# Kernel optimization log

Hardware: AMD Instinct MI355X
Metric: run time of the kernel (lower is better)

Reference implementation:

```python
import jax, jax.numpy as jnp
import numpy as np

IN_CH = 128
INTER = max(IN_CH // 8, 1)  # 16

def setup_inputs() -> dict:
    key = jax.random.key(0)
    ks = jax.random.split(key, 10)
    B, C, D, H, W = 2, IN_CH, 16, 24, 24
    s = 1.0 / np.sqrt(C)
    so = 1.0 / np.sqrt(INTER)
    return {
        "x":  jax.random.normal(ks[0], (B, C, D, H, W), dtype=jnp.float32),
        "Wq": jax.random.normal(ks[1], (INTER, C), dtype=jnp.float32) * s,
        "bq": jax.random.normal(ks[2], (INTER,), dtype=jnp.float32) * 0.01,
        "Wk": jax.random.normal(ks[3], (INTER, C), dtype=jnp.float32) * s,
        "bk": jax.random.normal(ks[4], (INTER,), dtype=jnp.float32) * 0.01,
        "Wv": jax.random.normal(ks[5], (INTER, C), dtype=jnp.float32) * s,
        "bv": jax.random.normal(ks[6], (INTER,), dtype=jnp.float32) * 0.01,
        "Wo": jax.random.normal(ks[7], (C, INTER), dtype=jnp.float32) * so,
        "bo": jax.random.normal(ks[8], (C,), dtype=jnp.float32) * 0.01,
        "gamma": jnp.zeros((1,), dtype=jnp.float32) + 0.5,  # nonzero so attn path is exercised
    }

def reference(x, Wq, bq, Wk, bk, Wv, bv, Wo, bo, gamma):
    B, C, D, H, W = x.shape
    N = D * H * W
    xf = x.reshape(B, C, N)  # flatten spatial
    # 1x1x1 conv == per-voxel channel matmul
    q = jnp.einsum('ic,bcn->bin', Wq, xf) + bq[None, :, None]  # [B,I,N]
    k = jnp.einsum('ic,bcn->bin', Wk, xf) + bk[None, :, None]
    v = jnp.einsum('ic,bcn->bin', Wv, xf) + bv[None, :, None]
    # attention[b,n,m] = sum_i q[b,i,n] k[b,i,m]; softmax over keys m
    attn = jax.nn.softmax(jnp.einsum('bin,bim->bnm', q, k), axis=-1)
    # out[b,c,n] = sum_m v[b,c,m] attn[b,n,m]
    out = jnp.einsum('bim,bnm->bin', v, attn)  # [B,I,N]
    out = jnp.einsum('ci,bin->bcn', Wo, out) + bo[None, :, None]
    out = out.reshape(B, C, D, H, W)
    return gamma[0] * out + x
```

## Files before the change

kernel.cpp:

```cpp
#include <hip/hip_runtime.h>

#define C_CH 128
#define I_CH 16
#define NVOX 9216
#define BATCH 2
#define LOG2E 1.44269504088896340736f

typedef unsigned short ushort_t;
typedef unsigned int uint_t;
typedef short bf16x8 __attribute__((ext_vector_type(8)));
typedef float f32x4 __attribute__((ext_vector_type(4)));

static __device__ inline ushort_t f2bf_rne(float x) {
    uint_t u = __builtin_bit_cast(uint_t, x);
    u = (u + 0x7FFFu + ((u >> 16) & 1u)) >> 16;
    return (ushort_t)u;
}

static __device__ inline float fast_exp2(float x) {
#if __has_builtin(__builtin_amdgcn_exp2f)
    return __builtin_amdgcn_exp2f(x);
#else
    return exp2f(x);
#endif
}

__global__ __launch_bounds__(256) void qkv_kernel(
    const float* __restrict__ x,
    const float* __restrict__ Wq, const float* __restrict__ bq,
    const float* __restrict__ Wk, const float* __restrict__ bk,
    const float* __restrict__ Wv, const float* __restrict__ bv,
    ushort_t* __restrict__ qb, ushort_t* __restrict__ kb,
    ushort_t* __restrict__ vT)
{
    __shared__ float xs[C_CH][64];
    __shared__ float ws[3][I_CH][C_CH];

    const int blk = blockIdx.x;
    const int b   = blk / (NVOX / 64);
    const int n0  = (blk % (NVOX / 64)) * 64;
    const int t   = threadIdx.x;

    {
        float4* wsq = (float4*)&ws[0][0][0];
        float4* wsk = (float4*)&ws[1][0][0];
        float4* wsv = (float4*)&ws[2][0][0];
        wsq[t]       = ((const float4*)Wq)[t];
        wsq[t + 256] = ((const float4*)Wq)[t + 256];
        wsk[t]       = ((const float4*)Wk)[t];
        wsk[t + 256] = ((const float4*)Wk)[t + 256];
        wsv[t]       = ((const float4*)Wv)[t];
        wsv[t + 256] = ((const float4*)Wv)[t + 256];
    }

    const float* xb = x + (size_t)b * C_CH * NVOX;
    #pragma unroll
    for (int rep = 0; rep < 8; ++rep) {
        int idx4 = rep * 256 + t;
        int c    = idx4 >> 4;
        int n4   = (idx4 & 15) << 2;
        *(float4*)&xs[c][n4] = *(const float4*)(xb + (size_t)c * NVOX + n0 + n4);
    }
    __syncthreads();

    const int n  = t & 63;
    const int iw = t >> 6;
    const int i0 = iw * 4;

    float aq[4] = {0.f,0.f,0.f,0.f};
    float ak[4] = {0.f,0.f,0.f,0.f};
    float av[4] = {0.f,0.f,0.f,0.f};

    #pragma unroll 2
    for (int c = 0; c < C_CH; c += 4) {
        float xv0 = xs[c + 0][n];
        float xv1 = xs[c + 1][n];
        float xv2 = xs[c + 2][n];
        float xv3 = xs[c + 3][n];
        #pragma unroll
        for (int j = 0; j < 4; ++j) {
            float4 w4;
            w4 = *(const float4*)&ws[0][i0 + j][c];
            aq[j] = fmaf(w4.x, xv0, fmaf(w4.y, xv1, fmaf(w4.z, xv2, fmaf(w4.w, xv3, aq[j]))));
            w4 = *(const float4*)&ws[1][i0 + j][c];
            ak[j] = fmaf(w4.x, xv0, fmaf(w4.y, xv1, fmaf(w4.z, xv2, fmaf(w4.w, xv3, ak[j]))));
            w4 = *(const float4*)&ws[2][i0 + j][c];
            av[j] = fmaf(w4.x, xv0, fmaf(w4.y, xv1, fmaf(w4.z, xv2, fmaf(w4.w, xv3, av[j]))));
        }
    }

    const size_t vox = (size_t)b * NVOX + n0 + n;
    ushort4 qv, kv;
    qv.x = f2bf_rne((aq[0] + bq[i0+0]) * LOG2E);
    qv.y = f2bf_rne((aq[1] + bq[i0+1]) * LOG2E);
    qv.z = f2bf_rne((aq[2] + bq[i0+2]) * LOG2E);
    qv.w = f2bf_rne((aq[3] + bq[i0+3]) * LOG2E);
    kv.x = f2bf_rne(ak[0] + bk[i0+0]); kv.y = f2bf_rne(ak[1] + bk[i0+1]);
    kv.z = f2bf_rne(ak[2] + bk[i0+2]); kv.w = f2bf_rne(ak[3] + bk[i0+3]);
    *(ushort4*)(qb + vox * I_CH + i0) = qv;
    *(ushort4*)(kb + vox * I_CH + i0) = kv;

    const int nl = n0 + n;
    #pragma unroll
    for (int j = 0; j < 4; ++j)
        vT[((size_t)b * I_CH + i0 + j) * NVOX + nl] = f2bf_rne(av[j] + bv[i0+j]);
}

__global__ __launch_bounds__(512) void attn_kernel(
    const ushort_t* __restrict__ qb, const ushort_t* __restrict__ kb,
    const ushort_t* __restrict__ vT,
    const float* __restrict__ Wo, const float* __restrict__ bo,
    const float* __restrict__ gamma, const float* __restrict__ x,
    float* __restrict__ out)
{
    __shared__ float po[4][32][18];
    __shared__ float lsh[8][33];
    __shared__ float aot[16][40];
    __shared__ float wo_s[C_CH][17];

    const int tid  = threadIdx.x;
    const int w    = tid >> 6;
    const int lane = tid & 63;
    const int l16  = lane & 15;
    const int quad = lane >> 4;

    {
        const int c  = tid >> 2;
        const int i4 = (tid & 3) * 4;
        float4 wv = *(const float4*)(Wo + c * I_CH + i4);
        wo_s[c][i4 + 0] = wv.x; wo_s[c][i4 + 1] = wv.y;
        wo_s[c][i4 + 2] = wv.z; wo_s[c][i4 + 3] = wv.w;
    }

    const int qvox0 = blockIdx.x * 32;
    const int b     = qvox0 / NVOX;
    const int nloc0 = qvox0 - b * NVOX;

    bf16x8 qf0 = (bf16x8)0, qf1 = (bf16x8)0;
    if (quad < 2) {
        qf0 = __builtin_bit_cast(bf16x8,
              *(const int4*)(qb + (size_t)(qvox0 + l16) * I_CH + quad * 8));
        qf1 = __builtin_bit_cast(bf16x8,
              *(const int4*)(qb + (size_t)(qvox0 + 16 + l16) * I_CH + quad * 8));
    }

    const int p0     = ((l16 >> 2) << 3) + (l16 & 3);
    const int mchunk = w * (NVOX / 8);
    const ushort_t* kp = kb + ((size_t)b * NVOX + mchunk + p0) * I_CH + (quad & 1) * 8;
    const ushort_t* vp = vT + ((size_t)b * I_CH + l16) * NVOX + mchunk + quad * 8;

    f32x4 O0 = {0.f,0.f,0.f,0.f}, O1 = {0.f,0.f,0.f,0.f};
    f32x4 L0 = {0.f,0.f,0.f,0.f}, L1 = {0.f,0.f,0.f,0.f};
    const f32x4 Z = {0.f,0.f,0.f,0.f};
    int4 onesi; onesi.x = onesi.y = onesi.z = onesi.w = 0x3F803F80;
    const bf16x8 ones = __builtin_bit_cast(bf16x8, onesi);

    for (int it = 0; it < NVOX / 8 / 64; ++it) {
        int4 ka0a = *(const int4*)(kp);
        int4 ka1a = *(const int4*)(kp + 4 * I_CH);
        int4 vaa  = *(const int4*)(vp);
        int4 ka0b = *(const int4*)(kp + 32 * I_CH);
        int4 ka1b = *(const int4*)(kp + 36 * I_CH);
        int4 vab  = *(const int4*)(vp + 32);
        kp += 64 * I_CH;
        vp += 64;

        f32x4 s00 = __builtin_amdgcn_mfma_f32_16x16x32_bf16(
            __builtin_bit_cast(bf16x8, ka0a), qf0, Z, 0, 0, 0);
        f32x4 s01 = __builtin_amdgcn_mfma_f32_16x16x32_bf16(
            __builtin_bit_cast(bf16x8, ka1a), qf0, Z, 0, 0, 0);
        f32x4 s10 = __builtin_amdgcn_mfma_f32_16x16x32_bf16(
            __builtin_bit_cast(bf16x8, ka0a), qf1, Z, 0, 0, 0);
        f32x4 s11 = __builtin_amdgcn_mfma_f32_16x16x32_bf16(
            __builtin_bit_cast(bf16x8, ka1a), qf1, Z, 0, 0, 0);

        f32x4 t00 = __builtin_amdgcn_mfma_f32_16x16x32_bf16(
            __builtin_bit_cast(bf16x8, ka0b), qf0, Z, 0, 0, 0);
        f32x4 t01 = __builtin_amdgcn_mfma_f32_16x16x32_bf16(
            __builtin_bit_cast(bf16x8, ka1b), qf0, Z, 0, 0, 0);
        f32x4 t10 = __builtin_amdgcn_mfma_f32_16x16x32_bf16(
            __builtin_bit_cast(bf16x8, ka0b), qf1, Z, 0, 0, 0);
        f32x4 t11 = __builtin_amdgcn_mfma_f32_16x16x32_bf16(
            __builtin_bit_cast(bf16x8, ka1b), qf1, Z, 0, 0, 0);

        {
            float p00 = fast_exp2(s00.x), p01 = fast_exp2(s00.y);
            float p02 = fast_exp2(s00.z), p03 = fast_exp2(s00.w);
            float p10 = fast_exp2(s01.x), p11 = fast_exp2(s01.y);
            float p12 = fast_exp2(s01.z), p13 = fast_exp2(s01.w);
            uint_t d0 = __builtin_amdgcn_perm(__builtin_bit_cast(uint_t, p01),
                                              __builtin_bit_cast(uint_t, p00), 0x07060302u);
            uint_t d1 = __builtin_amdgcn_perm(__builtin_bit_cast(uint_t, p03),
                                              __builtin_bit_cast(uint_t, p02), 0x07060302u);
            uint_t d2 = __builtin_amdgcn_perm(__builtin_bit_cast(uint_t, p11),
                                              __builtin_bit_cast(uint_t, p10), 0x07060302u);
            uint_t d3 = __builtin_amdgcn_perm(__builtin_bit_cast(uint_t, p13),
                                              __builtin_bit_cast(uint_t, p12), 0x07060302u);
            int4 pbi = make_int4((int)d0, (int)d1, (int)d2, (int)d3);
            bf16x8 pb = __builtin_bit_cast(bf16x8, pbi);
            O0 = __builtin_amdgcn_mfma_f32_16x16x32_bf16(
                __builtin_bit_cast(bf16x8, vaa), pb, O0, 0, 0, 0);
            L0 = __builtin_amdgcn_mfma_f32_16x16x32_bf16(ones, pb, L0, 0, 0, 0);
        }
        {
            float p00 = fast_exp2(s10.x), p01 = fast_exp2(s10.y);
            float p02 = fast_exp2(s10.z), p03 = fast_exp2(s10.w);
            float p10 = fast_exp2(s11.x), p11 = fast_exp2(s11.y);
            float p12 = fast_exp2(s11.z), p13 = fast_exp2(s11.w);
            uint_t d0 = __builtin_amdgcn_perm(__builtin_bit_cast(uint_t, p01),
                                              __builtin_bit_cast(uint_t, p00), 0x07060302u);
            uint_t d1 = __builtin_amdgcn_perm(__builtin_bit_cast(uint_t, p03),
                                              __builtin_bit_cast(uint_t, p02), 0x07060302u);
            uint_t d2 = __builtin_amdgcn_perm(__builtin_bit_cast(uint_t, p11),
                                              __builtin_bit_cast(uint_t, p10), 0x07060302u);
            uint_t d3 = __builtin_amdgcn_perm(__builtin_bit_cast(uint_t, p13),
                                              __builtin_bit_cast(uint_t, p12), 0x07060302u);
            int4 pbi = make_int4((int)d0, (int)d1, (int)d2, (int)d3);
            bf16x8 pb = __builtin_bit_cast(bf16x8, pbi);
            O1 = __builtin_amdgcn_mfma_f32_16x16x32_bf16(
                __builtin_bit_cast(bf16x8, vaa), pb, O1, 0, 0, 0);
            L1 = __builtin_amdgcn_mfma_f32_16x16x32_bf16(ones, pb, L1, 0, 0, 0);
        }
        {
            float p00 = fast_exp2(t00.x), p01 = fast_exp2(t00.y);
            float p02 = fast_exp2(t00.z), p03 = fast_exp2(t00.w);
            float p10 = fast_exp2(t01.x), p11 = fast_exp2(t01.y);
            float p12 = fast_exp2(t01.z), p13 = fast_exp2(t01.w);
            uint_t d0 = __builtin_amdgcn_perm(__builtin_bit_cast(uint_t, p01),
                                              __builtin_bit_cast(uint_t, p00), 0x07060302u);
            uint_t d1 = __builtin_amdgcn_perm(__builtin_bit_cast(uint_t, p03),
                                              __builtin_bit_cast(uint_t, p02), 0x07060302u);
            uint_t d2 = __builtin_amdgcn_perm(__builtin_bit_cast(uint_t, p11),
                                              __builtin_bit_cast(uint_t, p10), 0x07060302u);
            uint_t d3 = __builtin_amdgcn_perm(__builtin_bit_cast(uint_t, p13),
                                              __builtin_bit_cast(uint_t, p12), 0x07060302u);
            int4 pbi = make_int4((int)d0, (int)d1, (int)d2, (int)d3);
            bf16x8 pb = __builtin_bit_cast(bf16x8, pbi);
            O0 = __builtin_amdgcn_mfma_f32_16x16x32_bf16(
                __builtin_bit_cast(bf16x8, vab), pb, O0, 0, 0, 0);
            L0 = __builtin_amdgcn_mfma_f32_16x16x32_bf16(ones, pb, L0, 0, 0, 0);
        }
        {
            float p00 = fast_exp2(t10.x), p01 = fast_exp2(t10.y);
            float p02 = fast_exp2(t10.z), p03 = fast_exp2(t10.w);
            float p10 = fast_exp2(t11.x), p11 = fast_exp2(t11.y);
            float p12 = fast_exp2(t11.z), p13 = fast_exp2(t11.w);
            uint_t d0 = __builtin_amdgcn_perm(__builtin_bit_cast(uint_t, p01),
                                              __builtin_bit_cast(uint_t, p00), 0x07060302u);
            uint_t d1 = __builtin_amdgcn_perm(__builtin_bit_cast(uint_t, p03),
                                              __builtin_bit_cast(uint_t, p02), 0x07060302u);
            uint_t d2 = __builtin_amdgcn_perm(__builtin_bit_cast(uint_t, p11),
                                              __builtin_bit_cast(uint_t, p10), 0x07060302u);
            uint_t d3 = __builtin_amdgcn_perm(__builtin_bit_cast(uint_t, p13),
                                              __builtin_bit_cast(uint_t, p12), 0x07060302u);
            int4 pbi = make_int4((int)d0, (int)d1, (int)d2, (int)d3);
            bf16x8 pb = __builtin_bit_cast(bf16x8, pbi);
            O1 = __builtin_amdgcn_mfma_f32_16x16x32_bf16(
                __builtin_bit_cast(bf16x8, vab), pb, O1, 0, 0, 0);
            L1 = __builtin_amdgcn_mfma_f32_16x16x32_bf16(ones, pb, L1, 0, 0, 0);
        }
    }

    if (w < 4) {
        #pragma unroll
        for (int r = 0; r < 4; ++r) {
            po[w][quad * 4 + r][l16]      = O0[r];
            po[w][16 + quad * 4 + r][l16] = O1[r];
        }
    }
    if (quad == 0) { lsh[w][l16] = L0.x; lsh[w][16 + l16] = L1.x; }
    __syncthreads();

    if (w >= 4) {
        #pragma unroll
        for (int r = 0; r < 4; ++r) {
            po[w - 4][quad * 4 + r][l16]      += O0[r];
            po[w - 4][16 + quad * 4 + r][l16] += O1[r];
        }
    }
    __syncthreads();

    {
        const int q32 = tid & 31;
        const int i   = tid >> 5;
        const int row = (q32 >> 4) * 16 + i;
        const int col = q32 & 15;
        float v = 0.f, l = 0.f;
        #pragma unroll
        for (int ww = 0; ww < 4; ++ww) v += po[ww][row][col];
        #pragma unroll
        for (int ww = 0; ww < 8; ++ww) l += lsh[ww][q32];
        aot[i][q32] = v / l;
    }
    __syncthreads();

    const float g  = gamma[0];
    const int   c  = tid >> 2;
    const int   qh = (tid & 3) * 8;

    float acc[8];
    {
        const float b0 = bo[c];
        #pragma unroll
        for (int q = 0; q < 8; ++q) acc[q] = b0;
    }
    #pragma unroll
    for (int i = 0; i < 16; ++i) {
        const float wv = wo_s[c][i];
        float4 a0 = *(const float4*)&aot[i][qh];
        float4 a1 = *(const float4*)&aot[i][qh + 4];
        acc[0] = fmaf(wv, a0.x, acc[0]); acc[1] = fmaf(wv, a0.y, acc[1]);
        acc[2] = fmaf(wv, a0.z, acc[2]); acc[3] = fmaf(wv, a0.w, acc[3]);
        acc[4] = fmaf(wv, a1.x, acc[4]); acc[5] = fmaf(wv, a1.y, acc[5]);
        acc[6] = fmaf(wv, a1.z, acc[6]); acc[7] = fmaf(wv, a1.w, acc[7]);
    }

    const size_t gi = ((size_t)b * C_CH + c) * NVOX + nloc0 + qh;
    float4 x0 = *(const float4*)(x + gi);
    float4 x1 = *(const float4*)(x + gi + 4);
    float4 o0, o1;
    o0.x = fmaf(g, acc[0], x0.x); o0.y = fmaf(g, acc[1], x0.y);
    o0.z = fmaf(g, acc[2], x0.z); o0.w = fmaf(g, acc[3], x0.w);
    o1.x = fmaf(g, acc[4], x1.x); o1.y = fmaf(g, acc[5], x1.y);
    o1.z = fmaf(g, acc[6], x1.z); o1.w = fmaf(g, acc[7], x1.w);
    *(float4*)(out + gi)     = o0;
    *(float4*)(out + gi + 4) = o1;
}

extern "C" void kernel_launch(void* const* d_in, const int* in_sizes, int n_in,
                              void* d_out, int out_size, void* d_ws, size_t ws_size,
                              hipStream_t stream) {
    const float* x     = (const float*)d_in[0];
    const float* Wq    = (const float*)d_in[1];
    const float* bq    = (const float*)d_in[2];
    const float* Wk    = (const float*)d_in[3];
    const float* bk    = (const float*)d_in[4];
    const float* Wv    = (const float*)d_in[5];
    const float* bv    = (const float*)d_in[6];
    const float* Wo    = (const float*)d_in[7];
    const float* bo    = (const float*)d_in[8];
    const float* gamma = (const float*)d_in[9];
    float* out = (float*)d_out;

    ushort_t* qb = (ushort_t*)d_ws;
    ushort_t* kb = qb + (size_t)BATCH * NVOX * I_CH;
    ushort_t* vT = kb + (size_t)BATCH * NVOX * I_CH;

    hipLaunchKernelGGL(qkv_kernel, dim3(BATCH * NVOX / 64), dim3(256), 0, stream,
                       x, Wq, bq, Wk, bk, Wv, bv, qb, kb, vT);
    hipLaunchKernelGGL(attn_kernel, dim3(BATCH * NVOX / 32), dim3(512), 0, stream,
                       qb, kb, vT, Wo, bo, gamma, x, out);
}
```

Before: 130.0 us.

## Split key range across 16 waves and shrink QKV projection tiles

```diff
diff --git a/kernel.cpp b/kernel.cpp
--- a/kernel.cpp
+++ b/kernel.cpp
@@ -33,88 +33,70 @@
     ushort_t* __restrict__ qb, ushort_t* __restrict__ kb,
     ushort_t* __restrict__ vT)
 {
-    __shared__ float xs[C_CH][64];
-    __shared__ float ws[3][I_CH][C_CH];
-
-    const int blk = blockIdx.x;
-    const int b   = blk / (NVOX / 64);
-    const int n0  = (blk % (NVOX / 64)) * 64;
-    const int t   = threadIdx.x;
+    __shared__ float ws[3][I_CH][132];
+    __shared__ float xs[C_CH][I_CH];
+
+    const int t    = threadIdx.x;
+    const int vox0 = blockIdx.x * 16;
+    const int b    = vox0 / NVOX;
+    const int n0   = vox0 - b * NVOX;
 
     {
-        float4* wsq = (float4*)&ws[0][0][0];
-        float4* wsk = (float4*)&ws[1][0][0];
-        float4* wsv = (float4*)&ws[2][0][0];
-        wsq[t]       = ((const float4*)Wq)[t];
-        wsq[t + 256] = ((const float4*)Wq)[t + 256];
-        wsk[t]       = ((const float4*)Wk)[t];
-        wsk[t + 256] = ((const float4*)Wk)[t + 256];
-        wsv[t]       = ((const float4*)Wv)[t];
-        wsv[t + 256] = ((const float4*)Wv)[t + 256];
-    }
-
-    const float* xb = x + (size_t)b * C_CH * NVOX;
-    #pragma unroll
-    for (int rep = 0; rep < 8; ++rep) {
-        int idx4 = rep * 256 + t;
-        int c    = idx4 >> 4;
-        int n4   = (idx4 & 15) << 2;
-        *(float4*)&xs[c][n4] = *(const float4*)(xb + (size_t)c * NVOX + n0 + n4);
+        const int i  = t >> 4;
+        const int c8 = (t & 15) * 8;
+        const float4* wq4 = (const float4*)(Wq + i * C_CH + c8);
+        const float4* wk4 = (const float4*)(Wk + i * C_CH + c8);
+        const float4* wv4 = (const float4*)(Wv + i * C_CH + c8);
+        *(float4*)&ws[0][i][c8]     = wq4[0];
+        *(float4*)&ws[0][i][c8 + 4] = wq4[1];
+        *(float4*)&ws[1][i][c8]     = wk4[0];
+        *(float4*)&ws[1][i][c8 + 4] = wk4[1];
+        *(float4*)&ws[2][i][c8]     = wv4[0];
+        *(float4*)&ws[2][i][c8 + 4] = wv4[1];
+    }
+
+    {
+        const float* xb = x + (size_t)b * C_CH * NVOX + n0;
+        const int c   = t >> 2;
+        const int col = (t & 3) * 4;
+        *(float4*)&xs[c][col]      = *(const float4*)(xb + (size_t)c * NVOX + col);
+        *(float4*)&xs[c + 64][col] = *(const float4*)(xb + (size_t)(c + 64) * NVOX + col);
     }
     __syncthreads();
 
-    const int n  = t & 63;
-    const int iw = t >> 6;
-    const int i0 = iw * 4;
-
-    float aq[4] = {0.f,0.f,0.f,0.f};
-    float ak[4] = {0.f,0.f,0.f,0.f};
-    float av[4] = {0.f,0.f,0.f,0.f};
-
-    #pragma unroll 2
+    const int n = t & 15;
+    const int i = t >> 4;
+
+    float aq = 0.f, ak = 0.f, av = 0.f;
+    #pragma unroll 4
     for (int c = 0; c < C_CH; c += 4) {
-        float xv0 = xs[c + 0][n];
-        float xv1 = xs[c + 1][n];
-        float xv2 = xs[c + 2][n];
-        float xv3 = xs[c + 3][n];
-        #pragma unroll
-        for (int j = 0; j < 4; ++j) {
-            float4 w4;
-            w4 = *(const float4*)&ws[0][i0 + j][c];
-            aq[j] = fmaf(w4.x, xv0, fmaf(w4.y, xv1, fmaf(w4.z, xv2, fmaf(w4.w, xv3, aq[j]))));
-            w4 = *(const float4*)&ws[1][i0 + j][c];
-            ak[j] = fmaf(w4.x, xv0, fmaf(w4.y, xv1, fmaf(w4.z, xv2, fmaf(w4.w, xv3, ak[j]))));
-            w4 = *(const float4*)&ws[2][i0 + j][c];
-            av[j] = fmaf(w4.x, xv0, fmaf(w4.y, xv1, fmaf(w4.z, xv2, fmaf(w4.w, xv3, av[j]))));
-        }
-    }
-
-    const size_t vox = (size_t)b * NVOX + n0 + n;
-    ushort4 qv, kv;
-    qv.x = f2bf_rne((aq[0] + bq[i0+0]) * LOG2E);
-    qv.y = f2bf_rne((aq[1] + bq[i0+1]) * LOG2E);
-    qv.z = f2bf_rne((aq[2] + bq[i0+2]) * LOG2E);
-    qv.w = f2bf_rne((aq[3] + bq[i0+3]) * LOG2E);
-    kv.x = f2bf_rne(ak[0] + bk[i0+0]); kv.y = f2bf_rne(ak[1] + bk[i0+1]);
-    kv.z = f2bf_rne(ak[2] + bk[i0+2]); kv.w = f2bf_rne(ak[3] + bk[i0+3]);
-    *(ushort4*)(qb + vox * I_CH + i0) = qv;
-    *(ushort4*)(kb + vox * I_CH + i0) = kv;
-
-    const int nl = n0 + n;
-    #pragma unroll
-    for (int j = 0; j < 4; ++j)
-        vT[((size_t)b * I_CH + i0 + j) * NVOX + nl] = f2bf_rne(av[j] + bv[i0+j]);
-}
-
-__global__ __launch_bounds__(512) void attn_kernel(
+        float x0 = xs[c + 0][n];
+        float x1 = xs[c + 1][n];
+        float x2 = xs[c + 2][n];
+        float x3 = xs[c + 3][n];
+        float4 wq = *(const float4*)&ws[0][i][c];
+        float4 wk = *(const float4*)&ws[1][i][c];
+        float4 wv = *(const float4*)&ws[2][i][c];
+        aq = fmaf(wq.x, x0, fmaf(wq.y, x1, fmaf(wq.z, x2, fmaf(wq.w, x3, aq))));
+        ak = fmaf(wk.x, x0, fmaf(wk.y, x1, fmaf(wk.z, x2, fmaf(wk.w, x3, ak))));
+        av = fmaf(wv.x, x0, fmaf(wv.y, x1, fmaf(wv.z, x2, fmaf(wv.w, x3, av))));
+    }
+
+    const size_t vox = (size_t)vox0 + n;
+    qb[vox * I_CH + i] = f2bf_rne((aq + bq[i]) * LOG2E);
+    kb[vox * I_CH + i] = f2bf_rne(ak + bk[i]);
+    vT[((size_t)b * I_CH + i) * NVOX + n0 + n] = f2bf_rne(av + bv[i]);
+}
+
+__global__ __launch_bounds__(1024) void attn_kernel(
     const ushort_t* __restrict__ qb, const ushort_t* __restrict__ kb,
     const ushort_t* __restrict__ vT,
     const float* __restrict__ Wo, const float* __restrict__ bo,
     const float* __restrict__ gamma, const float* __restrict__ x,
     float* __restrict__ out)
 {
-    __shared__ float po[4][32][18];
-    __shared__ float lsh[8][33];
+    __shared__ float po[8][32][18];
+    __shared__ float lsh[16][33];
     __shared__ float aot[16][40];
     __shared__ float wo_s[C_CH][17];
 
@@ -124,7 +106,7 @@
     const int l16  = lane & 15;
     const int quad = lane >> 4;
 
-    {
+    if (tid < 512) {
         const int c  = tid >> 2;
         const int i4 = (tid & 3) * 4;
         float4 wv = *(const float4*)(Wo + c * I_CH + i4);
@@ -145,7 +127,7 @@
     }
 
     const int p0     = ((l16 >> 2) << 3) + (l16 & 3);
-    const int mchunk = w * (NVOX / 8);
+    const int mchunk = w * (NVOX / 16);
     const ushort_t* kp = kb + ((size_t)b * NVOX + mchunk + p0) * I_CH + (quad & 1) * 8;
     const ushort_t* vp = vT + ((size_t)b * I_CH + l16) * NVOX + mchunk + quad * 8;
 
@@ -155,7 +137,7 @@
     int4 onesi; onesi.x = onesi.y = onesi.z = onesi.w = 0x3F803F80;
     const bf16x8 ones = __builtin_bit_cast(bf16x8, onesi);
 
-    for (int it = 0; it < NVOX / 8 / 64; ++it) {
+    for (int it = 0; it < NVOX / 16 / 64; ++it) {
         int4 ka0a = *(const int4*)(kp);
         int4 ka1a = *(const int4*)(kp + 4 * I_CH);
         int4 vaa  = *(const int4*)(vp);
@@ -173,7 +155,6 @@
             __builtin_bit_cast(bf16x8, ka0a), qf1, Z, 0, 0, 0);
         f32x4 s11 = __builtin_amdgcn_mfma_f32_16x16x32_bf16(
             __builtin_bit_cast(bf16x8, ka1a), qf1, Z, 0, 0, 0);
-
         f32x4 t00 = __builtin_amdgcn_mfma_f32_16x16x32_bf16(
             __builtin_bit_cast(bf16x8, ka0b), qf0, Z, 0, 0, 0);
         f32x4 t01 = __builtin_amdgcn_mfma_f32_16x16x32_bf16(
@@ -261,7 +242,7 @@
         }
     }
 
-    if (w < 4) {
+    if (w < 8) {
         #pragma unroll
         for (int r = 0; r < 4; ++r) {
             po[w][quad * 4 + r][l16]      = O0[r];
@@ -271,60 +252,49 @@
     if (quad == 0) { lsh[w][l16] = L0.x; lsh[w][16 + l16] = L1.x; }
     __syncthreads();
 
-    if (w >= 4) {
+    if (w >= 8) {
         #pragma unroll
         for (int r = 0; r < 4; ++r) {
-            po[w - 4][quad * 4 + r][l16]      += O0[r];
-            po[w - 4][16 + quad * 4 + r][l16] += O1[r];
+            po[w - 8][quad * 4 + r][l16]      += O0[r];
+            po[w - 8][16 + quad * 4 + r][l16] += O1[r];
         }
     }
     __syncthreads();
 
-    {
+    if (tid < 512) {
         const int q32 = tid & 31;
         const int i   = tid >> 5;
         const int row = (q32 >> 4) * 16 + i;
         const int col = q32 & 15;
         float v = 0.f, l = 0.f;
         #pragma unroll
-        for (int ww = 0; ww < 4; ++ww) v += po[ww][row][col];
+        for (int ww = 0; ww < 8; ++ww) v += po[ww][row][col];
         #pragma unroll
-        for (int ww = 0; ww < 8; ++ww) l += lsh[ww][q32];
+        for (int ww = 0; ww < 16; ++ww) l += lsh[ww][q32];
         aot[i][q32] = v / l;
     }
     __syncthreads();
 
     const float g  = gamma[0];
-    const int   c  = tid >> 2;
-    const int   qh = (tid & 3) * 8;
-
-    float acc[8];
-    {
-        const float b0 = bo[c];
-        #pragma unroll
-        for (int q = 0; q < 8; ++q) acc[q] = b0;
-    }
+    const int   c  = tid >> 3;
+    const int   q4 = (tid & 7) * 4;
+
+    float4 acc;
+    acc.x = acc.y = acc.z = acc.w = bo[c];
     #pragma unroll
     for (int i = 0; i < 16; ++i) {
         const float wv = wo_s[c][i];
-        float4 a0 = *(const float4*)&aot[i][qh];
-        float4 a1 = *(const float4*)&aot[i][qh + 4];
-        acc[0] = fmaf(wv, a0.x, acc[0]); acc[1] = fmaf(wv, a0.y, acc[1]);
-        acc[2] = fmaf(wv, a0.z, acc[2]); acc[3] = fmaf(wv, a0.w, acc[3]);
-        acc[4] = fmaf(wv, a1.x, acc[4]); acc[5] = fmaf(wv, a1.y, acc[5]);
-        acc[6] = fmaf(wv, a1.z, acc[6]); acc[7] = fmaf(wv, a1.w, acc[7]);
-    }
-
-    const size_t gi = ((size_t)b * C_CH + c) * NVOX + nloc0 + qh;
-    float4 x0 = *(const float4*)(x + gi);
-    float4 x1 = *(const float4*)(x + gi + 4);
-    float4 o0, o1;
-    o0.x = fmaf(g, acc[0], x0.x); o0.y = fmaf(g, acc[1], x0.y);
-    o0.z = fmaf(g, acc[2], x0.z); o0.w = fmaf(g, acc[3], x0.w);
-    o1.x = fmaf(g, acc[4], x1.x); o1.y = fmaf(g, acc[5], x1.y);
-    o1.z = fmaf(g, acc[6], x1.z); o1.w = fmaf(g, acc[7], x1.w);
-    *(float4*)(out + gi)     = o0;
-    *(float4*)(out + gi + 4) = o1;
+        float4 a = *(const float4*)&aot[i][q4];
+        acc.x = fmaf(wv, a.x, acc.x); acc.y = fmaf(wv, a.y, acc.y);
+        acc.z = fmaf(wv, a.z, acc.z); acc.w = fmaf(wv, a.w, acc.w);
+    }
+
+    const size_t gi = ((size_t)b * C_CH + c) * NVOX + nloc0 + q4;
+    float4 xv = *(const float4*)(x + gi);
+    float4 ov;
+    ov.x = fmaf(g, acc.x, xv.x); ov.y = fmaf(g, acc.y, xv.y);
+    ov.z = fmaf(g, acc.z, xv.z); ov.w = fmaf(g, acc.w, xv.w);
+    *(float4*)(out + gi) = ov;
 }
 
 extern "C" void kernel_launch(void* const* d_in, const int* in_sizes, int n_in,
@@ -346,8 +316,8 @@
     ushort_t* kb = qb + (size_t)BATCH * NVOX * I_CH;
     ushort_t* vT = kb + (size_t)BATCH * NVOX * I_CH;
 
-    hipLaunchKernelGGL(qkv_kernel, dim3(BATCH * NVOX / 64), dim3(256), 0, stream,
+    hipLaunchKernelGGL(qkv_kernel, dim3(BATCH * NVOX / 16), dim3(256), 0, stream,
                        x, Wq, bq, Wk, bk, Wv, bv, qb, kb, vT);
-    hipLaunchKernelGGL(attn_kernel, dim3(BATCH * NVOX / 32), dim3(512), 0, stream,
+    hipLaunchKernelGGL(attn_kernel, dim3(BATCH * NVOX / 32), dim3(1024), 0, stream,
                        qb, kb, vT, Wo, bo, gamma, x, out);
 }
```

New measurement: 129.0 us. About the same (-0.8%).
